# Kernel optimization log

Hardware: AMD Instinct MI355X
Metric: run time of the kernel (lower is better)

The kernel has to match this reference:

```python
import jax, jax.numpy as jnp
import numpy as np

B, L, V, E, H, S = 64, 128, 100000, 300, 400, 50
HD = H // 2
START_IDX, END_IDX = S - 2, S - 1


def setup_inputs():
    key = jax.random.key(0)
    ks = jax.random.split(key, 10)
    words = jax.random.randint(ks[0], (B, L), 0, V)
    word_seq_lens = jnp.full((B,), L, dtype=jnp.int32)
    masks = jnp.ones((B, L), dtype=bool)
    tags = jax.random.randint(ks[1], (B, L), 0, S - 2)
    emb_table = jax.random.normal(ks[2], (V, E), dtype=jnp.float32) * 0.1
    lw = lambda k, shp: jax.random.normal(k, shp, dtype=jnp.float32) * 0.05
    w_ih_f = lw(ks[3], (4 * HD, E)); w_hh_f = lw(ks[4], (4 * HD, HD)); b_f = jnp.zeros((4 * HD,), jnp.float32)
    w_ih_b = lw(ks[5], (4 * HD, E)); w_hh_b = lw(ks[6], (4 * HD, HD)); b_b = jnp.zeros((4 * HD,), jnp.float32)
    W_tag = lw(ks[7], (S, H)); b_tag = jnp.zeros((S,), jnp.float32)
    transition = jax.random.normal(ks[8], (S, S), dtype=jnp.float32)
    transition = transition.at[:, START_IDX].set(-10000.0).at[END_IDX, :].set(-10000.0)
    return dict(words=words, word_seq_lens=word_seq_lens, masks=masks, tags=tags,
                emb_table=emb_table, w_ih_f=w_ih_f, w_hh_f=w_hh_f, b_f=b_f,
                w_ih_b=w_ih_b, w_hh_b=w_hh_b, b_b=b_b, W_tag=W_tag, b_tag=b_tag,
                transition=transition)


def _lstm_dir(x, w_ih, w_hh, b, reverse):
    # x: (B, L, D) -> (B, L, HD). PyTorch gate order: i, f, g, o.
    bsz = x.shape[0]
    xg = jnp.einsum('bld,gd->blg', x, w_ih) + b  # precompute input projections

    def step(carry, xt):
        h, c = carry
        g = xt + h @ w_hh.T
        i, f, gg, o = jnp.split(g, 4, axis=-1)
        c = jax.nn.sigmoid(f) * c + jax.nn.sigmoid(i) * jnp.tanh(gg)
        h = jax.nn.sigmoid(o) * jnp.tanh(c)
        return (h, c), h

    init = (jnp.zeros((bsz, HD), x.dtype), jnp.zeros((bsz, HD), x.dtype))
    _, hs = jax.lax.scan(step, init, jnp.swapaxes(xg, 0, 1), reverse=reverse)
    return jnp.swapaxes(hs, 0, 1)


def _forward_nll(words, word_seq_lens, masks, tags, emb_table,
                 w_ih_f, w_hh_f, b_f, w_ih_b, w_hh_b, b_b, W_tag, b_tag, transition):
    word_emb = emb_table[words]                              # (B, L, E); dropout = identity (eval)
    h_f = _lstm_dir(word_emb, w_ih_f, w_hh_f, b_f, reverse=False)
    h_b = _lstm_dir(word_emb, w_ih_b, w_hh_b, b_b, reverse=True)
    lstm_out = jnp.concatenate([h_f, h_b], axis=-1)          # (B, L, H)
    features = jnp.einsum('blh,sh->bls', lstm_out, W_tag) + b_tag  # (B, L, S)
    # all_scores[b,t,prev,cur] = transition[prev,cur] + features[b,t,cur]
    all_scores = transition[None, None] + features[:, :, None, :]  # (B, L, S, S)

    # ---- forward algorithm (unlabeled partition) ----
    alpha0 = all_scores[:, 0, START_IDX, :]                   # (B, S)

    def step(alpha, scores_t):
        alpha = jax.nn.logsumexp(alpha[:, :, None] + scores_t, axis=1)
        return alpha, alpha

    _, alphas_rest = jax.lax.scan(step, alpha0, jnp.swapaxes(all_scores[:, 1:], 0, 1))
    alphas = jnp.concatenate([alpha0[None], alphas_rest], axis=0)  # (L, B, S)
    alphas = jnp.swapaxes(alphas, 0, 1)                            # (B, L, S)
    last_alpha = jnp.take_along_axis(alphas, (word_seq_lens - 1)[:, None, None], axis=1)[:, 0]
    last_alpha = last_alpha + transition[:, END_IDX][None]
    unlabeled = jnp.sum(jax.nn.logsumexp(last_alpha, axis=1))

    # ---- gold path score (labeled) ----
    cur = jnp.take_along_axis(
        all_scores, jnp.broadcast_to(tags[:, :, None, None], (B, L, S, 1)), axis=3)[..., 0]  # (B, L, S)
    mid = jnp.take_along_axis(cur[:, 1:], tags[:, :L - 1, None], axis=2)[..., 0]             # (B, L-1)
    begin = cur[:, 0, START_IDX]
    end_tag_ids = jnp.take_along_axis(tags, (word_seq_lens - 1)[:, None], axis=1)[:, 0]
    end = transition[end_tag_ids, END_IDX]
    labeled = jnp.sum(begin) + jnp.sum(jnp.where(masks[:, 1:], mid, 0.0)) + jnp.sum(end)

    return unlabeled - labeled


def reference(words, word_seq_lens, masks, tags, emb_table, w_ih_f, w_hh_f, b_f,
              w_ih_b, w_hh_b, b_b, W_tag, b_tag, transition):
    return _forward_nll(words, word_seq_lens, masks, tags, emb_table,
                        w_ih_f, w_hh_f, b_f, w_ih_b, w_hh_b, b_b,
                        W_tag, b_tag, transition)
```

## Files before the change

### kernel.cpp

```cpp
#include <hip/hip_runtime.h>
#include <hip/hip_fp16.h>

#define B_ 64
#define L_ 128
#define E_ 300
#define HD_ 200
#define H_ 400
#define S_ 50
#define START_ 48
#define END_ 49
#define NG_ 1600
#define BL_ 8192

#define OFF_XG   0ull
#define OFF_LSTM 26214400ull
#define OFF_ABF  OFF_LSTM
#define OFF_BBF  (OFF_LSTM + 5242880ull)
#define OFF_SH   (OFF_LSTM + 13107200ull)
#define OFF_INV  (OFF_SH + 1638400ull)
#define OFF_WTB  (OFF_INV + 6400ull)
#define OFF_BIA  (OFF_WTB + 80000ull)
#define OFF_PART (OFF_BIA + 6400ull)

#define NA_T 2621440
#define NB_T 532480
#define PREP_BLOCKS 12427

typedef __attribute__((ext_vector_type(8))) short short8;
typedef __attribute__((ext_vector_type(4))) float f32x4;

__device__ __forceinline__ unsigned short f32_to_bf16(float f) {
    unsigned u = __float_as_uint(f);
    unsigned r = u + 0x7fffu + ((u >> 16) & 1u);
    return (unsigned short)(r >> 16);
}
__device__ __forceinline__ float bf16_to_f32(unsigned short s) {
    return __uint_as_float(((unsigned)s) << 16);
}
__device__ __forceinline__ int dot4(unsigned a, unsigned b, int c) {
#if __has_builtin(__builtin_amdgcn_sdot4)
    return __builtin_amdgcn_sdot4(a, b, c, false);
#else
    c += (int)(signed char)(a)       * (int)(signed char)(b);
    c += (int)(signed char)(a >> 8)  * (int)(signed char)(b >> 8);
    c += (int)(signed char)(a >> 16) * (int)(signed char)(b >> 16);
    c += (int)(signed char)(a >> 24) * (int)(signed char)(b >> 24);
    return c;
#endif
}
__device__ __forceinline__ float rlanef(float v, int l) {
#if __has_builtin(__builtin_amdgcn_readlane)
    return __uint_as_float(__builtin_amdgcn_readlane(__float_as_uint(v), l));
#else
    return __shfl(v, l, 64);
#endif
}

__global__ void prep_kernel(const int* __restrict__ words, const float* __restrict__ emb,
                            const float* __restrict__ wihf, const float* __restrict__ wihb,
                            const float* __restrict__ bfc, const float* __restrict__ bbc,
                            const float* __restrict__ wtag,
                            unsigned short* __restrict__ Abf, unsigned short* __restrict__ Bbf,
                            unsigned short* __restrict__ wtagB, float* __restrict__ biasC) {
    long g = (long)blockIdx.x * 256 + threadIdx.x;
    if (g < NA_T) {
        int i = (int)(g / 320), k = (int)(g % 320);
        float v = (k < E_) ? emb[(long)words[i] * E_ + k] : 0.f;
        Abf[g] = f32_to_bf16(v);
        return;
    }
    g -= NA_T;
    if (g < NB_T) {
        int r = (int)(g / 320), k = (int)(g % 320);
        float v = 0.f;
        if (r < NG_ && k < E_) v = (r < 800) ? wihf[r * E_ + k] : wihb[(r - 800) * E_ + k];
        Bbf[g] = f32_to_bf16(v);
        return;
    }
    g -= NB_T;
    if (g < 25600) {
        int s = (int)(g / 400), k = (int)(g % 400);
        float v = (s < S_) ? wtag[s * H_ + k] : 0.f;
        wtagB[g] = f32_to_bf16(v);
        return;
    }
    g -= 25600;
    if (g < 1600) { biasC[g] = (g < 800) ? bfc[g] : bbc[g - 800]; return; }
}

__global__ __launch_bounds__(256) void quant_kernel(const float* __restrict__ whh_f,
                                                    const float* __restrict__ whh_b,
                                                    signed char* __restrict__ w8,
                                                    float* __restrict__ invs) {
    int gw = (int)((blockIdx.x * 256 + threadIdx.x) >> 6);
    int lane = threadIdx.x & 63;
    if (gw >= 1600) return;
    int dir = gw / 800, row = gw % 800;
    const float* w = (dir ? whh_b : whh_f) + row * HD_;
    float m = 1e-20f;
    for (int k = lane; k < HD_; k += 64) m = fmaxf(m, fabsf(w[k]));
    for (int off = 32; off; off >>= 1) m = fmaxf(m, __shfl_xor(m, off));
    float s = 127.f / m;
    if (lane < 50) {
        int k0 = lane * 4;
        unsigned pk = 0;
#pragma unroll
        for (int i = 0; i < 4; ++i) {
            int v = (int)rintf(w[k0 + i] * s);
            pk |= ((unsigned)(v & 0xff)) << (8 * i);
        }
        unsigned char* base = (unsigned char*)w8 + dir * 160000;
        if (lane < 48) {
            int j = lane >> 2, wsel = lane & 3;
            *(unsigned*)(base + (size_t)(j * 800 + row) * 16 + wsel * 4) = pk;
        } else {
            *(unsigned*)(base + 153600 + (size_t)row * 8 + (lane - 48) * 4) = pk;
        }
    }
    if (lane == 0) invs[gw] = m / 16129.f;
}

__global__ __launch_bounds__(256) void xg_gemm(const unsigned short* __restrict__ Abf,
                                               const unsigned short* __restrict__ Bbf,
                                               const float* __restrict__ biasC,
                                               unsigned short* __restrict__ xg) {
    __shared__ unsigned short As[128 * 40];
    __shared__ unsigned short Bs[128 * 40];
    int tid = threadIdx.x;
    int bm = blockIdx.y * 128;
    int bn = blockIdx.x * 128;
    int srow = tid >> 1, half = tid & 1;
    int lane = tid & 63, wave = tid >> 6, r16 = lane & 15, kh = lane >> 4;

    f32x4 acc[2][8];
#pragma unroll
    for (int mi = 0; mi < 2; ++mi)
#pragma unroll
        for (int ni = 0; ni < 8; ++ni) acc[mi][ni] = (f32x4){0.f, 0.f, 0.f, 0.f};

    const unsigned short* Ar = Abf + (long)(bm + srow) * 320;
    const unsigned short* Br = Bbf + (long)(bn + srow) * 320;

    for (int k0 = 0; k0 < 320; k0 += 32) {
#pragma unroll
        for (int j = 0; j < 2; ++j) {
            int off = half * 16 + j * 8;
            *(uint4*)&As[srow * 40 + off] = *(const uint4*)(Ar + k0 + off);
            *(uint4*)&Bs[srow * 40 + off] = *(const uint4*)(Br + k0 + off);
        }
        __syncthreads();
        short8 af[2], bfv[8];
#pragma unroll
        for (int mi = 0; mi < 2; ++mi)
            af[mi] = *(const short8*)&As[(wave * 32 + mi * 16 + r16) * 40 + kh * 8];
#pragma unroll
        for (int ni = 0; ni < 8; ++ni)
            bfv[ni] = *(const short8*)&Bs[(ni * 16 + r16) * 40 + kh * 8];
#pragma unroll
        for (int mi = 0; mi < 2; ++mi)
#pragma unroll
            for (int ni = 0; ni < 8; ++ni)
                acc[mi][ni] = __builtin_amdgcn_mfma_f32_16x16x32_bf16(af[mi], bfv[ni], acc[mi][ni], 0, 0, 0);
        __syncthreads();
    }
#pragma unroll
    for (int ni = 0; ni < 8; ++ni) {
        int g = bn + ni * 16 + r16;
        if (g < NG_) {
            float bias = biasC[g];
#pragma unroll
            for (int mi = 0; mi < 2; ++mi) {
#pragma unroll
                for (int r = 0; r < 4; ++r) {
                    int row = bm + wave * 32 + mi * 16 + kh * 4 + r;
                    xg[(long)row * NG_ + g] = f32_to_bf16(acc[mi][ni][r] + bias);
                }
            }
        }
    }
}

__global__ __launch_bounds__(832) void lstm_rec(const unsigned short* __restrict__ xg,
                                                const signed char* __restrict__ w8,
                                                const float* __restrict__ invs,
                                                unsigned short* __restrict__ lstm16) {
    __shared__ __align__(16) unsigned char hbuf[256];
    __shared__ float a_lds[800];
    int tid = threadIdx.x;
    int dir = blockIdx.x >> 6;
    int b = blockIdx.x & 63;
    bool act = tid < 800;
    int tw = act ? tid : 0;
    int q = tid / 200;

    const unsigned char* wbase = (const unsigned char*)w8 + dir * 160000;
    uint4 wA[12];
    uint2 wAt;
#pragma unroll
    for (int j = 0; j < 12; ++j)
        wA[j] = *(const uint4*)(wbase + (size_t)(j * 800 + tw) * 16);
    wAt = *(const uint2*)(wbase + 153600 + (size_t)tw * 8);
#pragma unroll
    for (int j = 0; j < 12; ++j)
        asm volatile("" : "+v"(wA[j].x), "+v"(wA[j].y), "+v"(wA[j].z), "+v"(wA[j].w));
    asm volatile("" : "+v"(wAt.x), "+v"(wAt.y));

    float invsc = act ? invs[dir * 800 + tid] : 0.f;
    if (tid < 64) ((unsigned*)hbuf)[tid] = 0u;
    float c = 0.f;
    __syncthreads();

    const uint4* h4c = (const uint4*)hbuf;
    const uint2* ht2 = (const uint2*)(hbuf + 192);
    const unsigned short* xbase = xg + (long)b * L_ * NG_ + dir * 800;

    int t0 = dir ? (L_ - 1) : 0;
    float x = act ? bf16_to_f32(xbase[(long)t0 * NG_ + tid]) : 0.f;

    for (int step = 0; step < L_; ++step) {
        int t = dir ? (L_ - 1 - step) : step;
        float x_n = 0.f;
        if (act && step + 1 < L_) {
            int tn = dir ? (t - 1) : (t + 1);
            x_n = bf16_to_f32(xbase[(long)tn * NG_ + tid]);
        }
        if (act) {
            int di = 0;
#pragma unroll
            for (int j = 0; j < 12; ++j) {
                uint4 hh = h4c[j];
                di = dot4(wA[j].x, hh.x, di); di = dot4(wA[j].y, hh.y, di);
                di = dot4(wA[j].z, hh.z, di); di = dot4(wA[j].w, hh.w, di);
            }
            {
                uint2 hh = ht2[0];
                di = dot4(wAt.x, hh.x, di); di = dot4(wAt.y, hh.y, di);
            }
            float p = x + (float)di * invsc;
            float av;
            if (q == 2) {
                float e = __expf(-2.f * p);
                av = 2.f / (1.f + e) - 1.f;
            } else {
                av = 1.f / (1.f + __expf(-p));
            }
            a_lds[tid] = av;
        }
        __syncthreads();
        if (tid < HD_) {
            float ig = a_lds[tid];
            float fg = a_lds[200 + tid];
            float gg = a_lds[400 + tid];
            float og = a_lds[600 + tid];
            c = fg * c + ig * gg;
            float ec = __expf(-2.f * c);
            float hn = og * (2.f / (1.f + ec) - 1.f);
            ((signed char*)hbuf)[tid] = (signed char)(int)rintf(hn * 127.f);
            lstm16[((long)(b * L_ + t)) * H_ + dir * HD_ + tid] = f32_to_bf16(hn);
        }
        x = x_n;
        __syncthreads();
    }
}

__global__ __launch_bounds__(256) void feat_kernel(const unsigned short* __restrict__ lstm16,
                                                   const unsigned short* __restrict__ wtagB,
                                                   const float* __restrict__ btag,
                                                   float* __restrict__ feats) {
    __shared__ unsigned short As[128 * 40];
    __shared__ unsigned short Bs[64 * 40];
    int tid = threadIdx.x;
    int bm = blockIdx.x * 128;
    int srow = tid >> 1, half = tid & 1;
    int lane = tid & 63, wave = tid >> 6, r16 = lane & 15, kh = lane >> 4;

    f32x4 acc[2][4];
#pragma unroll
    for (int mi = 0; mi < 2; ++mi)
#pragma unroll
        for (int ni = 0; ni < 4; ++ni) acc[mi][ni] = (f32x4){0.f, 0.f, 0.f, 0.f};

    const unsigned short* Ar = lstm16 + (long)(bm + srow) * 400;
    const unsigned short* Br = wtagB + (long)srow * 400;

    for (int k0 = 0; k0 < 400; k0 += 32) {
#pragma unroll
        for (int j = 0; j < 2; ++j) {
            int off = half * 16 + j * 8;
            bool kv = (k0 + off + 8 <= 400);
            uint4 z = make_uint4(0u, 0u, 0u, 0u);
            *(uint4*)&As[srow * 40 + off] = kv ? *(const uint4*)(Ar + k0 + off) : z;
            if (srow < 64)
                *(uint4*)&Bs[srow * 40 + off] = kv ? *(const uint4*)(Br + k0 + off) : z;
        }
        __syncthreads();
        short8 af[2], bfv[4];
#pragma unroll
        for (int mi = 0; mi < 2; ++mi)
            af[mi] = *(const short8*)&As[(wave * 32 + mi * 16 + r16) * 40 + kh * 8];
#pragma unroll
        for (int ni = 0; ni < 4; ++ni)
            bfv[ni] = *(const short8*)&Bs[(ni * 16 + r16) * 40 + kh * 8];
#pragma unroll
        for (int mi = 0; mi < 2; ++mi)
#pragma unroll
            for (int ni = 0; ni < 4; ++ni)
                acc[mi][ni] = __builtin_amdgcn_mfma_f32_16x16x32_bf16(af[mi], bfv[ni], acc[mi][ni], 0, 0, 0);
        __syncthreads();
    }
#pragma unroll
    for (int ni = 0; ni < 4; ++ni) {
        int g = ni * 16 + r16;
        if (g < S_) {
            float bias = btag[g];
#pragma unroll
            for (int mi = 0; mi < 2; ++mi) {
#pragma unroll
                for (int r = 0; r < 4; ++r) {
                    int row = bm + wave * 32 + mi * 16 + kh * 4 + r;
                    feats[(long)row * S_ + g] = acc[mi][ni][r] + bias;
                }
            }
        }
    }
}

__global__ __launch_bounds__(64) void crf_kernel(const float* __restrict__ feats,
                                                 const float* __restrict__ trans,
                                                 const int* __restrict__ tags,
                                                 const int* __restrict__ seqlens,
                                                 float* __restrict__ part) {
    __shared__ float Tt[S_ * 53];
    __shared__ int tg[L_];
    int lane = threadIdx.x;
    int b = blockIdx.x;
    for (int idx = lane; idx < S_ * S_; idx += 64) {
        int j = idx / S_, i = idx % S_;
        Tt[j * 53 + i] = trans[i * S_ + j];
    }
    for (int idx = lane; idx < L_; idx += 64) tg[idx] = tags[b * L_ + idx];
    int slen = seqlens[b];
    const float* fb = feats + (long)b * L_ * S_;
    __syncthreads();

    bool act = lane < S_;
    const float* Trow = Tt + (act ? lane : 0) * 53;
    float alpha = act ? (Trow[START_] + fb[lane]) : -1e30f;
    float lal = alpha;

    for (int t = 1; t < L_; ++t) {
        const float* fbt = fb + t * S_;
        float fval = act ? fbt[lane] : 0.f;
        float m0 = -1e30f, m1 = -1e30f;
#pragma unroll
        for (int i = 0; i < S_; i += 2) {
            m0 = fmaxf(m0, rlanef(alpha, i) + Trow[i]);
            m1 = fmaxf(m1, rlanef(alpha, i + 1) + Trow[i + 1]);
        }
        float m = fmaxf(m0, m1);
        float s0 = 0.f, s1 = 0.f, s2 = 0.f, s3 = 0.f;
#pragma unroll
        for (int i = 0; i < S_; i += 4) {
            s0 += __expf(rlanef(alpha, i) + Trow[i] - m);
            s1 += __expf(rlanef(alpha, i + 1) + Trow[i + 1] - m);
            s2 += __expf(rlanef(alpha, i + 2) + Trow[i + 2] - m);
            s3 += __expf(rlanef(alpha, i + 3) + Trow[i + 3] - m);
        }
        float anew = m + __logf((s0 + s1) + (s2 + s3)) + fval;
        alpha = act ? anew : -1e30f;
        if (t == slen - 1) lal = alpha;
    }

    float la = act ? (lal + Tt[END_ * 53 + lane]) : -1e30f;
    float m = la;
    for (int off = 32; off; off >>= 1) m = fmaxf(m, __shfl_xor(m, off));
    float e = act ? __expf(la - m) : 0.f;
    for (int off = 32; off; off >>= 1) e += __shfl_xor(e, off);
    float unl = m + __logf(e);

    float lab = 0.f;
    for (int tt = lane; tt < L_; tt += 64) {
        if (tt == 0) {
            lab += Tt[tg[0] * 53 + START_] + fb[tg[0]];
        } else if (tt < slen) {
            lab += Tt[tg[tt] * 53 + tg[tt - 1]] + fb[tt * S_ + tg[tt]];
        }
    }
    if (lane == 0) lab += Tt[END_ * 53 + tg[slen - 1]];
    for (int off = 32; off; off >>= 1) lab += __shfl_xor(lab, off);
    if (lane == 0) part[b] = unl - lab;
}

__global__ void fin_kernel(const float* __restrict__ part, float* __restrict__ out) {
    float s = 0.f;
    for (int i = 0; i < B_; ++i) s += part[i];
    out[0] = s;
}

extern "C" void kernel_launch(void* const* d_in, const int* in_sizes, int n_in,
                              void* d_out, int out_size, void* d_ws, size_t ws_size,
                              hipStream_t stream) {
    const int*   words = (const int*)d_in[0];
    const int*   slens = (const int*)d_in[1];
    const int*   tags  = (const int*)d_in[3];
    const float* emb   = (const float*)d_in[4];
    const float* wihf  = (const float*)d_in[5];
    const float* whhf  = (const float*)d_in[6];
    const float* bf    = (const float*)d_in[7];
    const float* wihb  = (const float*)d_in[8];
    const float* whhb  = (const float*)d_in[9];
    const float* bb    = (const float*)d_in[10];
    const float* wtag  = (const float*)d_in[11];
    const float* btag  = (const float*)d_in[12];
    const float* trans = (const float*)d_in[13];

    char* ws = (char*)d_ws;
    unsigned short* xg     = (unsigned short*)(ws + OFF_XG);
    unsigned short* lstm16 = (unsigned short*)(ws + OFF_LSTM);
    unsigned short* Abf    = (unsigned short*)(ws + OFF_ABF);
    unsigned short* Bbf    = (unsigned short*)(ws + OFF_BBF);
    signed char*    w8     = (signed char*)(ws + OFF_SH);
    float*          fts    = (float*)(ws + OFF_SH);
    float*          invs   = (float*)(ws + OFF_INV);
    unsigned short* wtagB  = (unsigned short*)(ws + OFF_WTB);
    float*          biaC   = (float*)(ws + OFF_BIA);
    float*          part   = (float*)(ws + OFF_PART);
    float*          out    = (float*)d_out;

    prep_kernel<<<PREP_BLOCKS, 256, 0, stream>>>(words, emb, wihf, wihb, bf, bb,
                                                 wtag, Abf, Bbf, wtagB, biaC);
    quant_kernel<<<400, 256, 0, stream>>>(whhf, whhb, w8, invs);
    xg_gemm<<<dim3(13, 64), 256, 0, stream>>>(Abf, Bbf, biaC, xg);
    lstm_rec<<<128, 832, 0, stream>>>(xg, w8, invs, lstm16);
    feat_kernel<<<64, 256, 0, stream>>>(lstm16, wtagB, btag, fts);
    crf_kernel<<<64, 64, 0, stream>>>(fts, trans, tags, slens, part);
    fin_kernel<<<1, 1, 0, stream>>>(part, out);
}
```

Measured before the change: 314.7 us.

## Split LSTM recurrent weights across LDS, registers and L2; factor CRF logsumexp via exp(T)

The LSTM recurrence kernel now stages half of the int8 recurrent weights in shared memory and re-reads the other half from global memory (L2) each step, instead of holding all weights in registers. This frees registers for the 832-thread block, at the cost of extra LDS and global traffic in the serial loop. The CRF forward pass precomputes exp(transition) once and replaces the per-step max and exp over 50 terms with a wave max and 50 FMAs of exp(alpha - max) times exp(T). That removes about 50 exps per step but risks underflow when transitions are as low as -10000, which a clamp on the sum guards against.

Result: faster. 279.5 us (-11.2%).

```diff
diff --git a/kernel.cpp b/kernel.cpp
--- a/kernel.cpp
+++ b/kernel.cpp
@@ -184,6 +184,7 @@
                                                 const signed char* __restrict__ w8,
                                                 const float* __restrict__ invs,
                                                 unsigned short* __restrict__ lstm16) {
+    __shared__ __align__(16) uint4 wlds[4800];
     __shared__ __align__(16) unsigned char hbuf[256];
     __shared__ float a_lds[800];
     int tid = threadIdx.x;
@@ -194,16 +195,12 @@
     int q = tid / 200;
 
     const unsigned char* wbase = (const unsigned char*)w8 + dir * 160000;
-    uint4 wA[12];
-    uint2 wAt;
-#pragma unroll
-    for (int j = 0; j < 12; ++j)
-        wA[j] = *(const uint4*)(wbase + (size_t)(j * 800 + tw) * 16);
-    wAt = *(const uint2*)(wbase + 153600 + (size_t)tw * 8);
-#pragma unroll
-    for (int j = 0; j < 12; ++j)
-        asm volatile("" : "+v"(wA[j].x), "+v"(wA[j].y), "+v"(wA[j].z), "+v"(wA[j].w));
-    asm volatile("" : "+v"(wAt.x), "+v"(wAt.y));
+    {
+        const uint4* src = (const uint4*)wbase;
+        for (int i = tid; i < 4800; i += 832) wlds[i] = src[i];
+    }
+    const uint4* wstr = (const uint4*)wbase + 6 * 800 + tw;
+    const uint2* wtsr = (const uint2*)(wbase + 153600) + tw;
 
     float invsc = act ? invs[dir * 800 + tid] : 0.f;
     if (tid < 64) ((unsigned*)hbuf)[tid] = 0u;
@@ -219,6 +216,9 @@
 
     for (int step = 0; step < L_; ++step) {
         int t = dir ? (L_ - 1 - step) : step;
+        uint4 w6 = wstr[0], w7 = wstr[800], w8r = wstr[1600];
+        uint4 w9 = wstr[2400], w10 = wstr[3200], w11 = wstr[4000];
+        uint2 wt = wtsr[0];
         float x_n = 0.f;
         if (act && step + 1 < L_) {
             int tn = dir ? (t - 1) : (t + 1);
@@ -227,14 +227,28 @@
         if (act) {
             int di = 0;
 #pragma unroll
-            for (int j = 0; j < 12; ++j) {
+            for (int j = 0; j < 6; ++j) {
+                uint4 wv = wlds[j * 800 + tw];
                 uint4 hh = h4c[j];
-                di = dot4(wA[j].x, hh.x, di); di = dot4(wA[j].y, hh.y, di);
-                di = dot4(wA[j].z, hh.z, di); di = dot4(wA[j].w, hh.w, di);
+                di = dot4(wv.x, hh.x, di); di = dot4(wv.y, hh.y, di);
+                di = dot4(wv.z, hh.z, di); di = dot4(wv.w, hh.w, di);
             }
             {
-                uint2 hh = ht2[0];
-                di = dot4(wAt.x, hh.x, di); di = dot4(wAt.y, hh.y, di);
+                uint4 hh;
+                hh = h4c[6];  di = dot4(w6.x, hh.x, di);  di = dot4(w6.y, hh.y, di);
+                              di = dot4(w6.z, hh.z, di);  di = dot4(w6.w, hh.w, di);
+                hh = h4c[7];  di = dot4(w7.x, hh.x, di);  di = dot4(w7.y, hh.y, di);
+                              di = dot4(w7.z, hh.z, di);  di = dot4(w7.w, hh.w, di);
+                hh = h4c[8];  di = dot4(w8r.x, hh.x, di); di = dot4(w8r.y, hh.y, di);
+                              di = dot4(w8r.z, hh.z, di); di = dot4(w8r.w, hh.w, di);
+                hh = h4c[9];  di = dot4(w9.x, hh.x, di);  di = dot4(w9.y, hh.y, di);
+                              di = dot4(w9.z, hh.z, di);  di = dot4(w9.w, hh.w, di);
+                hh = h4c[10]; di = dot4(w10.x, hh.x, di); di = dot4(w10.y, hh.y, di);
+                              di = dot4(w10.z, hh.z, di); di = dot4(w10.w, hh.w, di);
+                hh = h4c[11]; di = dot4(w11.x, hh.x, di); di = dot4(w11.y, hh.y, di);
+                              di = dot4(w11.z, hh.z, di); di = dot4(w11.w, hh.w, di);
+                uint2 h2 = ht2[0];
+                di = dot4(wt.x, h2.x, di); di = dot4(wt.y, h2.y, di);
             }
             float p = x + (float)di * invsc;
             float av;
@@ -345,28 +359,29 @@
 
     bool act = lane < S_;
     const float* Trow = Tt + (act ? lane : 0) * 53;
+    float eT[S_];
+#pragma unroll
+    for (int i = 0; i < S_; ++i) eT[i] = __expf(Trow[i]);
+
     float alpha = act ? (Trow[START_] + fb[lane]) : -1e30f;
     float lal = alpha;
 
     for (int t = 1; t < L_; ++t) {
-        const float* fbt = fb + t * S_;
-        float fval = act ? fbt[lane] : 0.f;
-        float m0 = -1e30f, m1 = -1e30f;
-#pragma unroll
-        for (int i = 0; i < S_; i += 2) {
-            m0 = fmaxf(m0, rlanef(alpha, i) + Trow[i]);
-            m1 = fmaxf(m1, rlanef(alpha, i + 1) + Trow[i + 1]);
-        }
-        float m = fmaxf(m0, m1);
-        float s0 = 0.f, s1 = 0.f, s2 = 0.f, s3 = 0.f;
-#pragma unroll
-        for (int i = 0; i < S_; i += 4) {
-            s0 += __expf(rlanef(alpha, i) + Trow[i] - m);
-            s1 += __expf(rlanef(alpha, i + 1) + Trow[i + 1] - m);
-            s2 += __expf(rlanef(alpha, i + 2) + Trow[i + 2] - m);
-            s3 += __expf(rlanef(alpha, i + 3) + Trow[i + 3] - m);
-        }
-        float anew = m + __logf((s0 + s1) + (s2 + s3)) + fval;
+        float fval = act ? fb[t * S_ + lane] : 0.f;
+        float m = alpha;
+        for (int off = 32; off; off >>= 1) m = fmaxf(m, __shfl_xor(m, off));
+        float p = __expf(alpha - m);
+        float s0 = 0.f, s1 = 0.f, s2 = 0.f, s3 = 0.f, s4 = 0.f;
+#pragma unroll
+        for (int i = 0; i < S_; i += 5) {
+            s0 = fmaf(rlanef(p, i),     eT[i],     s0);
+            s1 = fmaf(rlanef(p, i + 1), eT[i + 1], s1);
+            s2 = fmaf(rlanef(p, i + 2), eT[i + 2], s2);
+            s3 = fmaf(rlanef(p, i + 3), eT[i + 3], s3);
+            s4 = fmaf(rlanef(p, i + 4), eT[i + 4], s4);
+        }
+        float s = fmaxf(((s0 + s1) + (s2 + s3)) + s4, 1e-38f);
+        float anew = m + __logf(s) + fval;
         alpha = act ? anew : -1e30f;
         if (t == slen - 1) lal = alpha;
     }
```

## Rewrite CRF forward recursion as exp-space matvec with precomputed exp(transition)

Applied to the files above, without the earlier changes.

Each lane now holds exp(transition row) in registers. Every timestep it computes exp(alpha - max) once, using a wave-wide max found by shuffles, and accumulates a dot product with FMAs. This replaces the per-element max pass and the fifty exps per step. The next step's emission is also prefetched to hide load latency. The cost is about fifty extra registers per lane, and the sum can underflow when transition entries are -10000; this is clamped with fmax(1e-38), which may change results when every path is masked.

Measured after the change: 263.6 us. -16.3%, faster.

```diff
diff --git a/kernel.cpp b/kernel.cpp
--- a/kernel.cpp
+++ b/kernel.cpp
@@ -345,30 +345,33 @@
 
     bool act = lane < S_;
     const float* Trow = Tt + (act ? lane : 0) * 53;
+    float eT[S_];
+#pragma unroll
+    for (int i = 0; i < S_; ++i) eT[i] = __expf(Trow[i]);
+
     float alpha = act ? (Trow[START_] + fb[lane]) : -1e30f;
     float lal = alpha;
+    float fval = act ? fb[S_ + lane] : 0.f;
 
     for (int t = 1; t < L_; ++t) {
-        const float* fbt = fb + t * S_;
-        float fval = act ? fbt[lane] : 0.f;
-        float m0 = -1e30f, m1 = -1e30f;
-#pragma unroll
-        for (int i = 0; i < S_; i += 2) {
-            m0 = fmaxf(m0, rlanef(alpha, i) + Trow[i]);
-            m1 = fmaxf(m1, rlanef(alpha, i + 1) + Trow[i + 1]);
-        }
-        float m = fmaxf(m0, m1);
-        float s0 = 0.f, s1 = 0.f, s2 = 0.f, s3 = 0.f;
-#pragma unroll
-        for (int i = 0; i < S_; i += 4) {
-            s0 += __expf(rlanef(alpha, i) + Trow[i] - m);
-            s1 += __expf(rlanef(alpha, i + 1) + Trow[i + 1] - m);
-            s2 += __expf(rlanef(alpha, i + 2) + Trow[i + 2] - m);
-            s3 += __expf(rlanef(alpha, i + 3) + Trow[i + 3] - m);
-        }
-        float anew = m + __logf((s0 + s1) + (s2 + s3)) + fval;
+        float fval_n = (act && t + 1 < L_) ? fb[(t + 1) * S_ + lane] : 0.f;
+        float m = alpha;
+        for (int off = 32; off; off >>= 1) m = fmaxf(m, __shfl_xor(m, off));
+        float p = __expf(alpha - m);
+        float s0 = 0.f, s1 = 0.f, s2 = 0.f, s3 = 0.f, s4 = 0.f;
+#pragma unroll
+        for (int i = 0; i < S_; i += 5) {
+            s0 = fmaf(rlanef(p, i),     eT[i],     s0);
+            s1 = fmaf(rlanef(p, i + 1), eT[i + 1], s1);
+            s2 = fmaf(rlanef(p, i + 2), eT[i + 2], s2);
+            s3 = fmaf(rlanef(p, i + 3), eT[i + 3], s3);
+            s4 = fmaf(rlanef(p, i + 4), eT[i + 4], s4);
+        }
+        float s = fmaxf(((s0 + s1) + (s2 + s3)) + s4, 1e-38f);
+        float anew = m + __logf(s) + fval;
         alpha = act ? anew : -1e30f;
         if (t == slen - 1) lal = alpha;
+        fval = fval_n;
     }
 
     float la = act ? (lal + Tt[END_ * 53 + lane]) : -1e30f;
```
